# Kernel optimization log

Hardware: AMD Instinct MI355X
Metric: run time of the kernel (lower is better)

Reference implementation:

```python
import jax, jax.numpy as jnp
import numpy as np

K_SIM_SCHEDULE = [4, 8, 16]
K_CON_SCHEDULE = [2, 4, 8]
NEG = 1000000000.0


def _dual_adjacency(h, k_sim, k_con):
    """Binary causal dual adjacency (similar / dissimilar), no gradient."""
    B, T, D = h.shape
    h = jax.lax.stop_gradient(h)
    xn = h / jnp.maximum(jnp.linalg.norm(h, axis=-1, keepdims=True), 1e-12)
    sim = jnp.einsum('btd,bsd->bts', xn, xn)                 # (B,T,T)
    past = jnp.tril(jnp.ones((T, T), h.dtype), -1)           # strictly-past mask
    sim = sim * past - NEG * (1.0 - past)
    eff_sim = min(k_sim, T - 1)
    eff_con = min(k_con, max(0, T - 1 - eff_sim))
    bI = jnp.arange(B)[:, None, None]
    tI = jnp.arange(T)[None, :, None]
    A_sim = jnp.zeros((B, T, T), h.dtype)
    if eff_sim > 0:
        _, top_idx = jax.lax.top_k(sim, eff_sim)             # (B,T,k)
        A_sim = A_sim.at[bI, tI, top_idx].set(1.0) * past
    A_con = jnp.zeros((B, T, T), h.dtype)
    if eff_con > 0:
        sim_con = jnp.where(A_sim > 0, NEG, sim)
        _, bot_idx = jax.lax.top_k(-sim_con, eff_con)        # smallest eff_con
        A_con = A_con.at[bI, tI, bot_idx].set(1.0) * past * (1.0 - A_sim)
    return A_sim, A_con


def _aggregate(h, A):
    # unweighted mean over selected neighbors; empty rows -> zeros
    deg = jnp.sum(A, axis=-1, keepdims=True)
    return jnp.einsum('bts,bsd->btd', A, h) / jnp.maximum(deg, 1.0)


def setup_inputs() -> dict:
    key = jax.random.key(0)
    ks = jax.random.split(key, 2)
    B, T, D, R = 4, 2048, 512, 3
    x = jax.random.normal(ks[0], (B, T, D), dtype=jnp.float32)
    gain = jnp.ones((R, D), dtype=jnp.float32)
    bias = jnp.zeros((R, D), dtype=jnp.float32)
    log_mix = jnp.zeros((R,), dtype=jnp.float32)
    log_alpha = jnp.zeros((R,), dtype=jnp.float32)
    log_momentum = jnp.asarray(1.0, dtype=jnp.float32)
    log_scale = jnp.asarray(0.0, dtype=jnp.float32)
    return {"x": x, "gain": gain, "bias": bias, "log_mix": log_mix,
            "log_alpha": log_alpha, "log_momentum": log_momentum,
            "log_scale": log_scale}


def reference(x, gain, bias, log_mix, log_alpha, log_momentum, log_scale):
    momentum = jax.nn.sigmoid(log_momentum)
    scale = jax.nn.softplus(log_scale) + 0.01
    h = x
    for r in range(len(K_SIM_SCHEDULE)):
        mix = jax.nn.sigmoid(log_mix[r])
        alpha = jax.nn.sigmoid(log_alpha[r])
        A_sim, A_con = _dual_adjacency(h, K_SIM_SCHEDULE[r], K_CON_SCHEDULE[r])
        msg_pos = _aggregate(h, A_sim)
        msg_neg = _aggregate(h, A_con)
        ctx = alpha * msg_pos + (1.0 - alpha) * msg_neg
        blended = mix * h + (1.0 - mix) * ctx
        h_new = jax.nn.gelu(blended * gain[r] + bias[r], approximate=False)
        h = momentum * h + (1.0 - momentum) * h_new
    return (h - x) * scale
```

## Files before the change

kernel.cpp:

```cpp
#include <hip/hip_runtime.h>
#include <hip/hip_bf16.h>
#include <cstdint>
#include <cstddef>

#define BB 4
#define TT 2048
#define DD 512
#define NEG_INF (-3.402823466e+38f)
#define POS_INF (3.402823466e+38f)

typedef __attribute__((ext_vector_type(8))) short bf16x8;
typedef __attribute__((ext_vector_type(8))) unsigned short ushort8;
typedef __attribute__((ext_vector_type(4))) float f32x4;

__device__ __forceinline__ float sigmoidf_(float x){ return 1.0f/(1.0f+expf(-x)); }

__device__ __forceinline__ unsigned short f2bf(float x){
  __hip_bfloat16 b = __float2bfloat16(x);
  return *reinterpret_cast<unsigned short*>(&b);
}

__device__ __forceinline__ unsigned int fwd_map(float f){
  unsigned int b = __float_as_uint(f);
  return b ^ ((b & 0x80000000u) ? 0xFFFFFFFFu : 0x80000000u);
}
__device__ __forceinline__ float inv_map(unsigned int u){
  unsigned int b = (u & 0x80000000u) ? (u ^ 0x80000000u) : ~u;
  return __uint_as_float(b);
}

__device__ __forceinline__ unsigned long long shfl_xor64(unsigned long long x, int off){
  unsigned int hi = __shfl_xor((unsigned int)(x >> 32), off);
  unsigned int lo = __shfl_xor((unsigned int)x, off);
  return ((unsigned long long)hi << 32) | lo;
}

__global__ __launch_bounds__(64) void k_normsplit(const float* __restrict__ h, float* __restrict__ rnorm,
                                                  unsigned short* __restrict__ Xh, unsigned short* __restrict__ Xl){
  int row = blockIdx.x;
  const float* hr = h + (size_t)row*DD;
  int lane = threadIdx.x;
  float4 v0 = *(const float4*)&hr[lane*4];
  float4 v1 = *(const float4*)&hr[lane*4 + 256];
  float ss = v0.x*v0.x+v0.y*v0.y+v0.z*v0.z+v0.w*v0.w
           + v1.x*v1.x+v1.y*v1.y+v1.z*v1.z+v1.w*v1.w;
  #pragma unroll
  for (int off=32; off; off>>=1) ss += __shfl_xor(ss, off);
  float rn = 1.0f / fmaxf(sqrtf(ss), 1e-12f);
  if (lane==0) rnorm[row] = rn;

  float xs[8] = {v0.x,v0.y,v0.z,v0.w,v1.x,v1.y,v1.z,v1.w};
  unsigned short hb[8], lb[8];
  #pragma unroll
  for (int q=0;q<8;q++){
    float xn = xs[q]*rn;
    unsigned short hh = f2bf(xn);
    __hip_bfloat16 bh = *reinterpret_cast<__hip_bfloat16*>(&hh);
    float rem = xn - __bfloat162float(bh);
    hb[q] = hh; lb[q] = f2bf(rem);
  }
  ushort4 h0 = {hb[0],hb[1],hb[2],hb[3]}, h1 = {hb[4],hb[5],hb[6],hb[7]};
  ushort4 l0 = {lb[0],lb[1],lb[2],lb[3]}, l1 = {lb[4],lb[5],lb[6],lb[7]};
  *(ushort4*)&Xh[(size_t)row*DD + lane*4]       = h0;
  *(ushort4*)&Xh[(size_t)row*DD + lane*4 + 256] = h1;
  *(ushort4*)&Xl[(size_t)row*DD + lane*4]       = l0;
  *(ushort4*)&Xl[(size_t)row*DD + lane*4 + 256] = l1;
}

__global__ __launch_bounds__(256) void k_sim(const unsigned short* __restrict__ Xh,
                                             const unsigned short* __restrict__ Xl,
                                             float* __restrict__ sim, int b0){
  int p = blockIdx.x;
  int jt = (int)((sqrtf(8.0f*(float)p + 1.0f) - 1.0f)*0.5f);
  while ((jt+1)*(jt+2)/2 <= p) jt++;
  while (jt*(jt+1)/2 > p) jt--;
  int is = p - jt*(jt+1)/2;

  int bl = blockIdx.y;
  size_t xoff = (size_t)(b0 + bl)*TT*DD;
  const unsigned short* XhB = Xh + xoff;
  const unsigned short* XlB = Xl + xoff;
  float* simb = sim + (size_t)bl*TT*TT;
  int t0 = jt*128, s0 = is*128;

  __shared__ __align__(16) short As[128*32];
  __shared__ __align__(16) short Bs[128*32];

  int tid = threadIdx.x, wave = tid>>6, lane = tid&63;
  int wr = wave>>1, wc = wave&1;

  int srow = tid>>2;
  int sc8  = (tid&3)*8;

  f32x4 acc[4][4];
  #pragma unroll
  for (int m=0;m<4;m++)
    #pragma unroll
    for (int n=0;n<4;n++) acc[m][n] = (f32x4){0.f,0.f,0.f,0.f};

  ushort8 ra0, ra1, rb0, rb1;
  auto gload = [&](int s){
    int pass = s>>4; int kcol = (s&15)*32;
    const unsigned short* sA = (pass<2) ? XhB : XlB;
    const unsigned short* sB = (pass!=1) ? XhB : XlB;
    ra0 = *(const ushort8*)&sA[(size_t)(t0+srow)*DD + kcol + sc8];
    ra1 = *(const ushort8*)&sA[(size_t)(t0+srow+64)*DD + kcol + sc8];
    rb0 = *(const ushort8*)&sB[(size_t)(s0+srow)*DD + kcol + sc8];
    rb1 = *(const ushort8*)&sB[(size_t)(s0+srow+64)*DD + kcol + sc8];
  };

  gload(0);
  for (int s=0; s<48; ++s){
    __syncthreads();
    *(ushort8*)&As[srow*32 + sc8]      = ra0;
    *(ushort8*)&As[(srow+64)*32 + sc8] = ra1;
    *(ushort8*)&Bs[srow*32 + sc8]      = rb0;
    *(ushort8*)&Bs[(srow+64)*32 + sc8] = rb1;
    __syncthreads();
    if (s < 47) gload(s+1);

    int arow = wr*64 + (lane&15);
    int brow = wc*64 + (lane&15);
    int kb = (lane>>4)*8;
    bf16x8 af[4], bf[4];
    #pragma unroll
    for (int m=0;m<4;m++) af[m] = *(const bf16x8*)&As[(arow + m*16)*32 + kb];
    #pragma unroll
    for (int n=0;n<4;n++) bf[n] = *(const bf16x8*)&Bs[(brow + n*16)*32 + kb];
    #pragma unroll
    for (int m=0;m<4;m++)
      #pragma unroll
      for (int n=0;n<4;n++)
        acc[m][n] = __builtin_amdgcn_mfma_f32_16x16x32_bf16(af[m], bf[n], acc[m][n], 0, 0, 0);
  }

  #pragma unroll
  for (int m=0;m<4;m++){
    int t = t0 + wr*64 + m*16 + (lane>>4)*4;
    #pragma unroll
    for (int n=0;n<4;n++){
      int sc = s0 + wc*64 + n*16 + (lane&15);
      float* dst = simb + (size_t)t*TT + sc;
      #pragma unroll
      for (int j=0;j<4;j++) dst[(size_t)j*TT] = acc[m][n][j];
    }
  }
}

#define BMASK 0xFFFFFF00u
#define MKKEY(F,S) ((((unsigned long long)fwd_map(F)) << 32) | (unsigned int)(~(S)))
#define INS(KK) do{ unsigned long long a=(KK); \
  if (a > kv3){ \
    if (a > kv0){ unsigned long long tq=kv0; kv0=a; a=tq; } \
    if (a > kv1){ unsigned long long tq=kv1; kv1=a; a=tq; } \
    if (a > kv2){ unsigned long long tq=kv2; kv2=a; a=tq; } \
    kv3=a; } }while(0)

__device__ __forceinline__ unsigned int radix24(const float* __restrict__ srow, int t, int k1,
                                                unsigned int flip, int* sh, int lane){
  #pragma unroll
  for (int i=0;i<4;i++) sh[lane + i*64] = 0;
  int t4 = t & ~3;
  for (int s4 = lane*4; s4 < t4; s4 += 256){
    float4 f = *(const float4*)&srow[s4];
    unsigned int u0=fwd_map(f.x)^flip, u1=fwd_map(f.y)^flip, u2=fwd_map(f.z)^flip, u3=fwd_map(f.w)^flip;
    atomicAdd(&sh[u0>>24],1); atomicAdd(&sh[u1>>24],1);
    atomicAdd(&sh[u2>>24],1); atomicAdd(&sh[u3>>24],1);
  }
  for (int s = t4 + lane; s < t; s += 64){
    unsigned int u = fwd_map(srow[s])^flip;
    atomicAdd(&sh[u>>24],1);
  }
  unsigned int pfx = 0u; int kp = k1;
  #pragma unroll
  for (int pass = 0; pass < 3; ++pass){
    int shift = 24 - 8*pass;
    int m4 = sh[4*lane] + sh[4*lane+1] + sh[4*lane+2] + sh[4*lane+3];
    int x = __shfl(m4, 63-lane);
    #pragma unroll
    for (int off = 1; off < 64; off <<= 1){
      int v = __shfl_up(x, off);
      if (lane >= off) x += v;
    }
    int T = __shfl(x, 63-lane);
    int G = T - m4;
    bool hit = (G < kp) && (kp <= T);
    unsigned int npfx = 0u; int nkp = 0;
    if (hit){
      int c = G; int D = 4*lane;
      #pragma unroll
      for (int i = 3; i >= 0; --i){
        int hc = sh[4*lane + i];
        if (kp <= c + hc){ D = 4*lane + i; break; }
        c += hc;
      }
      npfx = pfx | ((unsigned int)D << shift);
      nkp = kp - c;
    }
    unsigned long long hm = __ballot(hit);
    int src = __ffsll(hm) - 1;
    pfx = __shfl(npfx, src);
    kp  = __shfl(nkp, src);
    if (pass == 2) break;

    int nshift = shift - 8;
    unsigned int keep = 0xFFFFFFFFu << shift;
    #pragma unroll
    for (int i=0;i<4;i++) sh[lane + i*64] = 0;
    for (int s4 = lane*4; s4 < t4; s4 += 256){
      float4 f = *(const float4*)&srow[s4];
      unsigned int u0=fwd_map(f.x)^flip, u1=fwd_map(f.y)^flip, u2=fwd_map(f.z)^flip, u3=fwd_map(f.w)^flip;
      if (((u0 ^ pfx) & keep) == 0) atomicAdd(&sh[(u0>>nshift)&255],1);
      if (((u1 ^ pfx) & keep) == 0) atomicAdd(&sh[(u1>>nshift)&255],1);
      if (((u2 ^ pfx) & keep) == 0) atomicAdd(&sh[(u2>>nshift)&255],1);
      if (((u3 ^ pfx) & keep) == 0) atomicAdd(&sh[(u3>>nshift)&255],1);
    }
    for (int s = t4 + lane; s < t; s += 64){
      unsigned int u = fwd_map(srow[s])^flip;
      if (((u ^ pfx) & keep) == 0) atomicAdd(&sh[(u>>nshift)&255],1);
    }
  }
  return pfx;
}

template<int ESIM, int ECON>
__global__ __launch_bounds__(256) void k_topk(const float* __restrict__ sim, int b0,
                                              const float* __restrict__ h, const float* __restrict__ rnorm,
                                              int* __restrict__ topidx, int* __restrict__ botidx,
                                              int* __restrict__ bcnt){
  constexpr int K1  = ESIM + 8;
  constexpr int K1B = ESIM + ECON + 8;
  constexpr int CANDCAP = 40;
  constexpr int EQCAP = 44;
  constexpr float TAU = 5e-5f;
  __shared__ int s_hist[4][256];
  __shared__ int s_cand[4][CANDCAP];
  __shared__ int s_eq[4][EQCAP];
  __shared__ int s_sel[4][ESIM];
  __shared__ int s_bot[4][16];
  __shared__ int s_cnt[4][2];

  int tid = threadIdx.x, lane = tid & 63, wid = tid >> 6;
  int lrow = blockIdx.x*4 + wid;
  int bl = lrow >> 11, t = lrow & (TT-1);
  int gb = b0 + bl;
  int grow = (gb << 11) | t;

  if (t <= ESIM){
    if (lane < t) topidx[(size_t)grow*16 + lane] = lane;
    if (lane == 0) bcnt[grow] = 0;
    return;
  }
  const float* srow = sim + (size_t)lrow*TT;
  const float* hb  = h + (size_t)gb*TT*DD;
  const float* rnb = rnorm + (size_t)gb*TT;

  int* sh    = s_hist[wid];
  int* scand = s_cand[wid];
  int* seq   = s_eq[wid];
  int* ssel  = s_sel[wid];
  int* sbot  = s_bot[wid];
  int t4 = t & ~3;

  unsigned long long kv0=0, kv1=0, kv2=0, kv3=0;
  {
    int s4 = lane*4;
    for (; s4 + 772 <= t4; s4 += 1024){
      float4 f0 = *(const float4*)&srow[s4];
      float4 f1 = *(const float4*)&srow[s4+256];
      float4 f2 = *(const float4*)&srow[s4+512];
      float4 f3 = *(const float4*)&srow[s4+768];
      INS(MKKEY(f0.x,s4));     INS(MKKEY(f0.y,s4+1));   INS(MKKEY(f0.z,s4+2));   INS(MKKEY(f0.w,s4+3));
      INS(MKKEY(f1.x,s4+256)); INS(MKKEY(f1.y,s4+257)); INS(MKKEY(f1.z,s4+258)); INS(MKKEY(f1.w,s4+259));
      INS(MKKEY(f2.x,s4+512)); INS(MKKEY(f2.y,s4+513)); INS(MKKEY(f2.z,s4+514)); INS(MKKEY(f2.w,s4+515));
      INS(MKKEY(f3.x,s4+768)); INS(MKKEY(f3.y,s4+769)); INS(MKKEY(f3.z,s4+770)); INS(MKKEY(f3.w,s4+771));
    }
    for (; s4 < t4; s4 += 256){
      float4 f = *(const float4*)&srow[s4];
      INS(MKKEY(f.x,s4)); INS(MKKEY(f.y,s4+1)); INS(MKKEY(f.z,s4+2)); INS(MKKEY(f.w,s4+3));
    }
    for (int s = t4 + lane; s < t; s += 64) INS(MKKEY(srow[s],s));
  }

  unsigned long long cert = kv3;
  #pragma unroll
  for (int off=32; off; off>>=1){
    unsigned long long oc = shfl_xor64(cert, off);
    if (oc > cert) cert = oc;
  }

  int myidx = 0x7fffffff;
  float vA = 0.f, vB = 0.f;
  unsigned long long keyLast = 0ull;
  #pragma unroll
  for (int k = 0; k <= ESIM; ++k){
    unsigned long long bk = kv0;
    #pragma unroll
    for (int off=32; off; off>>=1){
      unsigned long long ok = shfl_xor64(bk, off);
      if (ok > bk) bk = ok;
    }
    if (kv0 == bk){ kv0=kv1; kv1=kv2; kv2=kv3; kv3=0ull; }
    if (lane == k) myidx = (int)(~(unsigned int)bk);
    if (k == ESIM-1) vA = inv_map((unsigned int)(bk >> 32));
    if (k == ESIM){ vB = inv_map((unsigned int)(bk >> 32)); keyLast = bk; }
  }

  bool fb = (cert > keyLast) || (vA - vB < TAU);
  if (!fb){
    if (lane < ESIM){
      ssel[lane] = myidx;
      topidx[(size_t)grow*16 + lane] = myidx;
    }
  } else {
    int k1 = min(t, K1);
    unsigned int thr = radix24(srow, t, k1, 0u, sh, lane);

    if (lane == 0){ s_cnt[wid][0] = 0; s_cnt[wid][1] = 0; }
    for (int s4 = lane*4; s4 < t4; s4 += 256){
      float4 f = *(const float4*)&srow[s4];
      unsigned int uu[4] = {fwd_map(f.x), fwd_map(f.y), fwd_map(f.z), fwd_map(f.w)};
      #pragma unroll
      for (int q=0;q<4;q++){
        unsigned int b24 = uu[q] & BMASK;
        if (b24 > thr){ int p = atomicAdd(&s_cnt[wid][0],1); if (p < CANDCAP) scand[p] = s4+q; }
        else if (b24 == thr){ int p = atomicAdd(&s_cnt[wid][1],1); if (p < EQCAP) seq[p] = s4+q; }
      }
    }
    for (int s = t4 + lane; s < t; s += 64){
      unsigned int b24 = fwd_map(srow[s]) & BMASK;
      if (b24 > thr){ int p = atomicAdd(&s_cnt[wid][0],1); if (p < CANDCAP) scand[p] = s; }
      else if (b24 == thr){ int p = atomicAdd(&s_cnt[wid][1],1); if (p < EQCAP) seq[p] = s; }
    }
    int c_gt = min(s_cnt[wid][0], CANDCAP);
    int c_eq = min(s_cnt[wid][1], EQCAP);
    int ncand = min(c_gt + c_eq, 64);

    unsigned int myu = 0u; int myi = 0x7fffffff;
    if (lane < ncand){
      myi = (lane < c_gt) ? scand[lane] : seq[lane - c_gt];
      myu = fwd_map(srow[myi]);
    }

    float fvA = 0.f, fvB = 0.f;
    {
      unsigned int cu = myu; int ci = myi;
      #pragma unroll
      for (int k = 0; k <= ESIM; ++k){
        unsigned int bu = cu; int bi = ci;
        #pragma unroll
        for (int off=32; off; off>>=1){
          unsigned int ou = __shfl_xor(bu, off); int oi = __shfl_xor(bi, off);
          if (ou > bu || (ou == bu && oi < bi)){ bu = ou; bi = oi; }
        }
        if (k < ESIM && lane == 0) ssel[k] = bi;
        if (k == ESIM-1) fvA = inv_map(bu);
        if (k == ESIM)   fvB = inv_map(bu);
        if (ci == bi){ cu = 0u; ci = 0x7fffffff; }
      }
    }

    bool resc = (fvA - fvB < TAU);
    if (resc){
      const float* hq = hb + (size_t)t*DD;
      float rt = rnb[t];
      float4 q0 = *(const float4*)&hq[lane*4];
      float4 q1 = *(const float4*)&hq[lane*4 + 256];
      float ev = NEG_INF;
      for (int j = 0; j < ncand; ++j){
        int idx = (j < c_gt) ? scand[j] : seq[j - c_gt];
        const float* hc = hb + (size_t)idx*DD;
        float4 c0 = *(const float4*)&hc[lane*4];
        float4 c1 = *(const float4*)&hc[lane*4 + 256];
        float pp = q0.x*c0.x+q0.y*c0.y+q0.z*c0.z+q0.w*c0.w
                 + q1.x*c1.x+q1.y*c1.y+q1.z*c1.z+q1.w*c1.w;
        #pragma unroll
        for (int off=32; off; off>>=1) pp += __shfl_xor(pp, off);
        float ex = pp * rt * rnb[idx];
        if (lane == j) ev = ex;
      }
      float rv = (lane < ncand) ? ev : NEG_INF;
      int   ri = myi;
      #pragma unroll
      for (int k = 0; k < ESIM; ++k){
        float bv = rv; int bi = ri;
        #pragma unroll
        for (int off=32; off; off>>=1){
          float ov = __shfl_xor(bv, off); int oi = __shfl_xor(bi, off);
          if (ov > bv || (ov == bv && oi < bi)){ bv = ov; bi = oi; }
        }
        if (lane == 0) ssel[k] = bi;
        if (ri == bi) rv = NEG_INF;
      }
    }
    if (lane < ESIM) topidx[(size_t)grow*16 + lane] = ssel[lane];
  }

  int need = ECON - (TT - t);
  int cnt2 = 0;
  if (need > 0){
    constexpr unsigned int FLIP = 0xFFFFFFFFu;
    int k1b = min(t, K1B);
    unsigned int thrb = radix24(srow, t, k1b, FLIP, sh, lane);

    if (lane == 0){ s_cnt[wid][0] = 0; s_cnt[wid][1] = 0; }
    for (int s4 = lane*4; s4 < t4; s4 += 256){
      float4 f = *(const float4*)&srow[s4];
      unsigned int uu[4] = {fwd_map(f.x)^FLIP, fwd_map(f.y)^FLIP, fwd_map(f.z)^FLIP, fwd_map(f.w)^FLIP};
      #pragma unroll
      for (int q=0;q<4;q++){
        unsigned int b24 = uu[q] & BMASK;
        if (b24 > thrb){ int p = atomicAdd(&s_cnt[wid][0],1); if (p < CANDCAP) scand[p] = s4+q; }
        else if (b24 == thrb){ int p = atomicAdd(&s_cnt[wid][1],1); if (p < EQCAP) seq[p] = s4+q; }
      }
    }
    for (int s = t4 + lane; s < t; s += 64){
      unsigned int u = fwd_map(srow[s])^FLIP;
      unsigned int b24 = u & BMASK;
      if (b24 > thrb){ int p = atomicAdd(&s_cnt[wid][0],1); if (p < CANDCAP) scand[p] = s; }
      else if (b24 == thrb){ int p = atomicAdd(&s_cnt[wid][1],1); if (p < EQCAP) seq[p] = s; }
    }
    int bc_gt = min(s_cnt[wid][0], CANDCAP);
    int bc_eq = min(s_cnt[wid][1], EQCAP);
    int ncb = min(bc_gt + bc_eq, 64);

    unsigned int mu = 0u; int mi = 0x7fffffff;
    if (lane < ncb){
      mi = (lane < bc_gt) ? scand[lane] : seq[lane - bc_gt];
      mu = fwd_map(srow[mi]) ^ FLIP;
    }
    float wA = 0.f, wB = 0.f;
    unsigned int cu = mu; int ci = mi;
    #pragma unroll
    for (int k = 0; k < K1B; ++k){
      if (k < ncb && cnt2 < need + 8){
        unsigned int bu = cu; int bi = ci;
        #pragma unroll
        for (int off=32; off; off>>=1){
          unsigned int ou = __shfl_xor(bu, off); int oi = __shfl_xor(bi, off);
          if (ou > bu || (ou == bu && oi < bi)){ bu = ou; bi = oi; }
        }
        if (ci == bi){ cu = 0u; ci = 0x7fffffff; }
        bool mem = false;
        #pragma unroll
        for (int j=0;j<ESIM;j++) if (ssel[j] == bi) mem = true;
        if (!mem){
          if (lane == 0) sbot[cnt2] = bi;
          float val = inv_map(bu ^ FLIP);
          if (cnt2 == need-1) wA = val;
          if (cnt2 == need)   wB = val;
          cnt2++;
        }
      }
    }
    int npick = min(need, cnt2);
    bool rb = (cnt2 > need) && (wB - wA < TAU);
    if (!rb){
      if (lane < npick) botidx[(size_t)grow*8 + lane] = sbot[lane];
    } else {
      const float* hq = hb + (size_t)t*DD;
      float rt = rnb[t];
      float4 q0 = *(const float4*)&hq[lane*4];
      float4 q1 = *(const float4*)&hq[lane*4 + 256];
      float ev = POS_INF; int ei = 0x7fffffff;
      for (int j = 0; j < cnt2; ++j){
        int idx = sbot[j];
        const float* hc = hb + (size_t)idx*DD;
        float4 c0 = *(const float4*)&hc[lane*4];
        float4 c1 = *(const float4*)&hc[lane*4 + 256];
        float pp = q0.x*c0.x+q0.y*c0.y+q0.z*c0.z+q0.w*c0.w
                 + q1.x*c1.x+q1.y*c1.y+q1.z*c1.z+q1.w*c1.w;
        #pragma unroll
        for (int off=32; off; off>>=1) pp += __shfl_xor(pp, off);
        float ex = pp * rt * rnb[idx];
        if (lane == j){ ev = ex; ei = idx; }
      }
      #pragma unroll
      for (int k = 0; k < ECON; ++k){
        if (k < npick){
          float bv = ev; int bi = ei;
          #pragma unroll
          for (int off=32; off; off>>=1){
            float ov = __shfl_xor(bv, off); int oi = __shfl_xor(bi, off);
            if (ov < bv || (ov == bv && oi < bi)){ bv = ov; bi = oi; }
          }
          if (lane == 0) botidx[(size_t)grow*8 + k] = bi;
          if (ei == bi) ev = POS_INF;
        }
      }
    }
    cnt2 = npick;
  }
  if (lane == 0) bcnt[grow] = cnt2;
}

__global__ __launch_bounds__(256) void k_agg(const float* __restrict__ hsrc, float* __restrict__ hdst,
                                             const int* __restrict__ topidx, const int* __restrict__ botidx,
                                             const int* __restrict__ bcnt,
                                             const float* __restrict__ gain, const float* __restrict__ bias,
                                             const float* __restrict__ log_mix, const float* __restrict__ log_alpha,
                                             const float* __restrict__ log_momentum, int r, int eff_sim){
  int row = blockIdx.x;
  int b = row >> 11; int t = row & (TT-1);
  int n_sim = min(eff_sim, t);
  int n_con = bcnt[row];
  float mix      = sigmoidf_(log_mix[r]);
  float alpha    = sigmoidf_(log_alpha[r]);
  float momentum = sigmoidf_(log_momentum[0]);
  const float* hb = hsrc + (size_t)b*TT*DD;

  __shared__ int sidx[16];
  __shared__ int scidx[8];
  if (threadIdx.x < 16) sidx[threadIdx.x]  = (threadIdx.x < n_sim) ? topidx[(size_t)row*16 + threadIdx.x] : 0;
  if (threadIdx.x < 8)  scidx[threadIdx.x] = (threadIdx.x < n_con) ? botidx[(size_t)row*8  + threadIdx.x] : 0;
  __syncthreads();

  #pragma unroll
  for (int e = threadIdx.x; e < DD; e += 256){
    float sp = 0.f;
    for (int j=0;j<n_sim;j++) sp += hb[(size_t)sidx[j]*DD + e];
    float sn = 0.f;
    for (int j=0;j<n_con;j++) sn += hb[(size_t)scidx[j]*DD + e];
    float mp = sp / (float)max(n_sim, 1);
    float mn = sn / (float)max(n_con, 1);
    float ctx = alpha*mp + (1.f-alpha)*mn;
    float hv = hsrc[(size_t)row*DD + e];
    float blended = mix*hv + (1.f-mix)*ctx;
    float u = blended*gain[e] + bias[e];
    float g = 0.5f*u*(1.0f + erff(u*0.7071067811865475f));
    hdst[(size_t)row*DD + e] = momentum*hv + (1.f-momentum)*g;
  }
}

__global__ __launch_bounds__(256) void k_final(const float* __restrict__ hfin, const float* __restrict__ x,
                                               const float* __restrict__ log_scale, float* __restrict__ out, int n){
  float scale = log1pf(expf(log_scale[0])) + 0.01f;
  int i = blockIdx.x*256 + threadIdx.x;
  if (i < n) out[i] = (hfin[i] - x[i]) * scale;
}

extern "C" void kernel_launch(void* const* d_in, const int* in_sizes, int n_in,
                              void* d_out, int out_size, void* d_ws, size_t ws_size,
                              hipStream_t stream) {
  const float* x         = (const float*)d_in[0];
  const float* gain      = (const float*)d_in[1];
  const float* bias      = (const float*)d_in[2];
  const float* log_mix   = (const float*)d_in[3];
  const float* log_alpha = (const float*)d_in[4];
  const float* log_mom   = (const float*)d_in[5];
  const float* log_scale = (const float*)d_in[6];

  float* hA = (float*)d_out;
  char* ws = (char*)d_ws;
  size_t off = 0;
  auto alloc = [&](size_t bytes){ void* p = ws + off; off += (bytes + 255) & ~(size_t)255; return p; };

  float*          hB     = (float*)alloc((size_t)BB*TT*DD*4);
  float*          rnorm  = (float*)alloc((size_t)BB*TT*4);
  int*            topidx = (int*)  alloc((size_t)BB*TT*16*4);
  int*            botidx = (int*)  alloc((size_t)BB*TT*8*4);
  int*            bcnt   = (int*)  alloc((size_t)BB*TT*4);
  unsigned short* Xh     = (unsigned short*)alloc((size_t)BB*TT*DD*2);
  unsigned short* Xl     = (unsigned short*)alloc((size_t)BB*TT*DD*2);

  size_t rem = (ws_size > off) ? (ws_size - off) : 0;
  int cb = (int)(rem / ((size_t)TT*TT*4));
  if (cb < 1) cb = 1;
  if (cb > BB) cb = BB;
  float* sim = (float*)alloc((size_t)cb*TT*TT*4);

  const float* hsrc = x;
  float* hdst = hB;
  const int ks[3] = {4, 8, 16};

  for (int r = 0; r < 3; ++r){
    k_normsplit<<<BB*TT, 64, 0, stream>>>(hsrc, rnorm, Xh, Xl);
    for (int b0 = 0; b0 < BB; b0 += cb){
      int nb = (BB - b0 < cb) ? (BB - b0) : cb;
      dim3 g(136, nb);
      k_sim<<<g, 256, 0, stream>>>(Xh, Xl, sim, b0);
      if (r == 0)      k_topk<4,2><<<nb*TT/4, 256, 0, stream>>>(sim, b0, hsrc, rnorm, topidx, botidx, bcnt);
      else if (r == 1) k_topk<8,4><<<nb*TT/4, 256, 0, stream>>>(sim, b0, hsrc, rnorm, topidx, botidx, bcnt);
      else             k_topk<16,8><<<nb*TT/4, 256, 0, stream>>>(sim, b0, hsrc, rnorm, topidx, botidx, bcnt);
    }
    k_agg<<<BB*TT, 256, 0, stream>>>(hsrc, hdst, topidx, botidx, bcnt,
                                     gain + (size_t)r*DD, bias + (size_t)r*DD,
                                     log_mix, log_alpha, log_mom, r, ks[r]);
    if (r == 0){ hsrc = hB; hdst = hA; }
    else if (r == 1){ hsrc = hA; hdst = hB; }
  }
  k_final<<<(BB*TT*DD)/256, 256, 0, stream>>>(hB, x, log_scale, (float*)d_out, BB*TT*DD);
}
```

Baseline: 462.4 us.

## Emit 16-bit sort keys from sim kernel and prefilter top-k on them

Measured after the change: 467.3 us. About the same (+1.1%).

```diff
diff --git a/kernel.cpp b/kernel.cpp
--- a/kernel.cpp
+++ b/kernel.cpp
@@ -69,7 +69,8 @@
 
 __global__ __launch_bounds__(256) void k_sim(const unsigned short* __restrict__ Xh,
                                              const unsigned short* __restrict__ Xl,
-                                             float* __restrict__ sim, int b0){
+                                             float* __restrict__ sim,
+                                             unsigned short* __restrict__ keys, int b0){
   int p = blockIdx.x;
   int jt = (int)((sqrtf(8.0f*(float)p + 1.0f) - 1.0f)*0.5f);
   while ((jt+1)*(jt+2)/2 <= p) jt++;
@@ -81,6 +82,7 @@
   const unsigned short* XhB = Xh + xoff;
   const unsigned short* XlB = Xl + xoff;
   float* simb = sim + (size_t)bl*TT*TT;
+  unsigned short* keyb = keys + (size_t)bl*TT*TT;
   int t0 = jt*128, s0 = is*128;
 
   __shared__ __align__(16) short As[128*32];
@@ -141,20 +143,32 @@
     for (int n=0;n<4;n++){
       int sc = s0 + wc*64 + n*16 + (lane&15);
       float* dst = simb + (size_t)t*TT + sc;
-      #pragma unroll
-      for (int j=0;j<4;j++) dst[(size_t)j*TT] = acc[m][n][j];
+      unsigned short* kdst = keyb + (size_t)t*TT + sc;
+      #pragma unroll
+      for (int j=0;j<4;j++){
+        float v = acc[m][n][j];
+        dst[(size_t)j*TT] = v;
+        kdst[(size_t)j*TT] = (unsigned short)(fwd_map(v) >> 16);
+      }
     }
   }
 }
 
 #define BMASK 0xFFFFFF00u
-#define MKKEY(F,S) ((((unsigned long long)fwd_map(F)) << 32) | (unsigned int)(~(S)))
-#define INS(KK) do{ unsigned long long a=(KK); \
-  if (a > kv3){ \
-    if (a > kv0){ unsigned long long tq=kv0; kv0=a; a=tq; } \
-    if (a > kv1){ unsigned long long tq=kv1; kv1=a; a=tq; } \
-    if (a > kv2){ unsigned long long tq=kv2; kv2=a; a=tq; } \
-    kv3=a; } }while(0)
+
+#define KLO(D,S) ( ((D) << 16)         | (0x7FFu - (unsigned int)(S)) )
+#define KHI(D,S) ( ((D) & 0xFFFF0000u) | (0x7FFu - (unsigned int)(S)) )
+#define INS32(KK) do{ unsigned int a=(KK); \
+  if (a > kv3){ unsigned int d0=kv3; if (d0 > cert) cert = d0; \
+    if (a > kv0){ unsigned int q=kv0; kv0=a; a=q; } \
+    if (a > kv1){ unsigned int q=kv1; kv1=a; a=q; } \
+    if (a > kv2){ unsigned int q=kv2; kv2=a; a=q; } \
+    kv3=a; } \
+  else { if (a > cert) cert = a; } }while(0)
+#define PROC8(W,S) { INS32(KLO((W).x,(S)));   INS32(KHI((W).x,(S)+1)); \
+                     INS32(KLO((W).y,(S)+2)); INS32(KHI((W).y,(S)+3)); \
+                     INS32(KLO((W).z,(S)+4)); INS32(KHI((W).z,(S)+5)); \
+                     INS32(KLO((W).w,(S)+6)); INS32(KHI((W).w,(S)+7)); }
 
 __device__ __forceinline__ unsigned int radix24(const float* __restrict__ srow, int t, int k1,
                                                 unsigned int flip, int* sh, int lane){
@@ -224,7 +238,8 @@
 }
 
 template<int ESIM, int ECON>
-__global__ __launch_bounds__(256) void k_topk(const float* __restrict__ sim, int b0,
+__global__ __launch_bounds__(256) void k_topk(const float* __restrict__ sim,
+                                              const unsigned short* __restrict__ keys, int b0,
                                               const float* __restrict__ h, const float* __restrict__ rnorm,
                                               int* __restrict__ topidx, int* __restrict__ botidx,
                                               int* __restrict__ bcnt){
@@ -252,6 +267,7 @@
     return;
   }
   const float* srow = sim + (size_t)lrow*TT;
+  const unsigned short* krow = keys + (size_t)lrow*TT;
   const float* hb  = h + (size_t)gb*TT*DD;
   const float* rnb = rnorm + (size_t)gb*TT;
 
@@ -262,31 +278,55 @@
   int* sbot  = s_bot[wid];
   int t4 = t & ~3;
 
-  unsigned long long kv0=0, kv1=0, kv2=0, kv3=0;
+  unsigned int kv0=0, kv1=0, kv2=0, kv3=0, cert=0;
   {
-    int s4 = lane*4;
-    for (; s4 + 772 <= t4; s4 += 1024){
-      float4 f0 = *(const float4*)&srow[s4];
-      float4 f1 = *(const float4*)&srow[s4+256];
-      float4 f2 = *(const float4*)&srow[s4+512];
-      float4 f3 = *(const float4*)&srow[s4+768];
-      INS(MKKEY(f0.x,s4));     INS(MKKEY(f0.y,s4+1));   INS(MKKEY(f0.z,s4+2));   INS(MKKEY(f0.w,s4+3));
-      INS(MKKEY(f1.x,s4+256)); INS(MKKEY(f1.y,s4+257)); INS(MKKEY(f1.z,s4+258)); INS(MKKEY(f1.w,s4+259));
-      INS(MKKEY(f2.x,s4+512)); INS(MKKEY(f2.y,s4+513)); INS(MKKEY(f2.z,s4+514)); INS(MKKEY(f2.w,s4+515));
-      INS(MKKEY(f3.x,s4+768)); INS(MKKEY(f3.y,s4+769)); INS(MKKEY(f3.z,s4+770)); INS(MKKEY(f3.w,s4+771));
-    }
-    for (; s4 < t4; s4 += 256){
-      float4 f = *(const float4*)&srow[s4];
-      INS(MKKEY(f.x,s4)); INS(MKKEY(f.y,s4+1)); INS(MKKEY(f.z,s4+2)); INS(MKKEY(f.w,s4+3));
-    }
-    for (int s = t4 + lane; s < t; s += 64) INS(MKKEY(srow[s],s));
-  }
-
-  unsigned long long cert = kv3;
+    int nd  = t >> 1;
+    int nd4 = nd >> 2;
+    const uint4* kr4 = (const uint4*)krow;
+    uint4 w0, w1, w2, w3;
+    bool g0 = (lane       < nd4);
+    bool g1 = (lane +  64 < nd4);
+    bool g2 = (lane + 128 < nd4);
+    bool g3 = (lane + 192 < nd4);
+    if (g0) w0 = kr4[lane];
+    if (g1) w1 = kr4[lane + 64];
+    if (g2) w2 = kr4[lane + 128];
+    if (g3) w3 = kr4[lane + 192];
+    if (g0) PROC8(w0, (lane)*8);
+    if (g1) PROC8(w1, (lane+64)*8);
+    if (g2) PROC8(w2, (lane+128)*8);
+    if (g3) PROC8(w3, (lane+192)*8);
+    for (int d = nd4*4 + lane; d < nd; d += 64){
+      unsigned int w = ((const unsigned int*)krow)[d];
+      int s = 2*d;
+      INS32(KLO(w, s)); INS32(KHI(w, s+1));
+    }
+    if ((t & 1) && lane == 0){
+      unsigned int u16 = krow[t-1];
+      INS32((u16 << 16) | (0x7FFu - (unsigned int)(t-1)));
+    }
+  }
   #pragma unroll
   for (int off=32; off; off>>=1){
-    unsigned long long oc = shfl_xor64(cert, off);
+    unsigned int oc = __shfl_xor(cert, off);
     if (oc > cert) cert = oc;
+  }
+
+  unsigned long long q0=0, q1=0, q2=0, q3=0;
+  {
+    int s0i = 0x7FF - (int)(kv0 & 0xFFFFu);
+    int s1i = 0x7FF - (int)(kv1 & 0xFFFFu);
+    int s2i = 0x7FF - (int)(kv2 & 0xFFFFu);
+    int s3i = 0x7FF - (int)(kv3 & 0xFFFFu);
+    float f0=0.f, f1=0.f, f2=0.f, f3=0.f;
+    if (kv0) f0 = srow[s0i];
+    if (kv1) f1 = srow[s1i];
+    if (kv2) f2 = srow[s2i];
+    if (kv3) f3 = srow[s3i];
+    if (kv0) q0 = (((unsigned long long)fwd_map(f0)) << 32) | (unsigned int)(~s0i);
+    if (kv1) q1 = (((unsigned long long)fwd_map(f1)) << 32) | (unsigned int)(~s1i);
+    if (kv2) q2 = (((unsigned long long)fwd_map(f2)) << 32) | (unsigned int)(~s2i);
+    if (kv3) q3 = (((unsigned long long)fwd_map(f3)) << 32) | (unsigned int)(~s3i);
   }
 
   int myidx = 0x7fffffff;
@@ -294,19 +334,20 @@
   unsigned long long keyLast = 0ull;
   #pragma unroll
   for (int k = 0; k <= ESIM; ++k){
-    unsigned long long bk = kv0;
+    unsigned long long bk = q0;
     #pragma unroll
     for (int off=32; off; off>>=1){
       unsigned long long ok = shfl_xor64(bk, off);
       if (ok > bk) bk = ok;
     }
-    if (kv0 == bk){ kv0=kv1; kv1=kv2; kv2=kv3; kv3=0ull; }
+    if (q0 == bk){ q0=q1; q1=q2; q2=q3; q3=0ull; }
     if (lane == k) myidx = (int)(~(unsigned int)bk);
     if (k == ESIM-1) vA = inv_map((unsigned int)(bk >> 32));
     if (k == ESIM){ vB = inv_map((unsigned int)(bk >> 32)); keyLast = bk; }
   }
 
-  bool fb = (cert > keyLast) || (vA - vB < TAU);
+  unsigned int k16Last = (unsigned int)(keyLast >> 48);
+  bool fb = ((cert >> 16) >= k16Last) || (vA - vB < TAU);
   if (!fb){
     if (lane < ESIM){
       ssel[lane] = myidx;
@@ -364,16 +405,16 @@
     if (resc){
       const float* hq = hb + (size_t)t*DD;
       float rt = rnb[t];
-      float4 q0 = *(const float4*)&hq[lane*4];
-      float4 q1 = *(const float4*)&hq[lane*4 + 256];
+      float4 qq0 = *(const float4*)&hq[lane*4];
+      float4 qq1 = *(const float4*)&hq[lane*4 + 256];
       float ev = NEG_INF;
       for (int j = 0; j < ncand; ++j){
         int idx = (j < c_gt) ? scand[j] : seq[j - c_gt];
         const float* hc = hb + (size_t)idx*DD;
         float4 c0 = *(const float4*)&hc[lane*4];
         float4 c1 = *(const float4*)&hc[lane*4 + 256];
-        float pp = q0.x*c0.x+q0.y*c0.y+q0.z*c0.z+q0.w*c0.w
-                 + q1.x*c1.x+q1.y*c1.y+q1.z*c1.z+q1.w*c1.w;
+        float pp = qq0.x*c0.x+qq0.y*c0.y+qq0.z*c0.z+qq0.w*c0.w
+                 + qq1.x*c1.x+qq1.y*c1.y+qq1.z*c1.z+qq1.w*c1.w;
         #pragma unroll
         for (int off=32; off; off>>=1) pp += __shfl_xor(pp, off);
         float ex = pp * rt * rnb[idx];
@@ -460,16 +501,16 @@
     } else {
       const float* hq = hb + (size_t)t*DD;
       float rt = rnb[t];
-      float4 q0 = *(const float4*)&hq[lane*4];
-      float4 q1 = *(const float4*)&hq[lane*4 + 256];
+      float4 qq0 = *(const float4*)&hq[lane*4];
+      float4 qq1 = *(const float4*)&hq[lane*4 + 256];
       float ev = POS_INF; int ei = 0x7fffffff;
       for (int j = 0; j < cnt2; ++j){
         int idx = sbot[j];
         const float* hc = hb + (size_t)idx*DD;
         float4 c0 = *(const float4*)&hc[lane*4];
         float4 c1 = *(const float4*)&hc[lane*4 + 256];
-        float pp = q0.x*c0.x+q0.y*c0.y+q0.z*c0.z+q0.w*c0.w
-                 + q1.x*c1.x+q1.y*c1.y+q1.z*c1.z+q1.w*c1.w;
+        float pp = qq0.x*c0.x+qq0.y*c0.y+qq0.z*c0.z+qq0.w*c0.w
+                 + qq1.x*c1.x+qq1.y*c1.y+qq1.z*c1.z+qq1.w*c1.w;
         #pragma unroll
         for (int off=32; off; off>>=1) pp += __shfl_xor(pp, off);
         float ex = pp * rt * rnb[idx];
@@ -564,10 +605,11 @@
   unsigned short* Xl     = (unsigned short*)alloc((size_t)BB*TT*DD*2);
 
   size_t rem = (ws_size > off) ? (ws_size - off) : 0;
-  int cb = (int)(rem / ((size_t)TT*TT*4));
+  int cb = (int)(rem / ((size_t)TT*TT*6 + 512));
   if (cb < 1) cb = 1;
   if (cb > BB) cb = BB;
-  float* sim = (float*)alloc((size_t)cb*TT*TT*4);
+  float*          sim  = (float*)alloc((size_t)cb*TT*TT*4);
+  unsigned short* keys = (unsigned short*)alloc((size_t)cb*TT*TT*2);
 
   const float* hsrc = x;
   float* hdst = hB;
@@ -578,10 +620,10 @@
     for (int b0 = 0; b0 < BB; b0 += cb){
       int nb = (BB - b0 < cb) ? (BB - b0) : cb;
       dim3 g(136, nb);
-      k_sim<<<g, 256, 0, stream>>>(Xh, Xl, sim, b0);
-      if (r == 0)      k_topk<4,2><<<nb*TT/4, 256, 0, stream>>>(sim, b0, hsrc, rnorm, topidx, botidx, bcnt);
-      else if (r == 1) k_topk<8,4><<<nb*TT/4, 256, 0, stream>>>(sim, b0, hsrc, rnorm, topidx, botidx, bcnt);
-      else             k_topk<16,8><<<nb*TT/4, 256, 0, stream>>>(sim, b0, hsrc, rnorm, topidx, botidx, bcnt);
+      k_sim<<<g, 256, 0, stream>>>(Xh, Xl, sim, keys, b0);
+      if (r == 0)      k_topk<4,2><<<nb*TT/4, 256, 0, stream>>>(sim, keys, b0, hsrc, rnorm, topidx, botidx, bcnt);
+      else if (r == 1) k_topk<8,4><<<nb*TT/4, 256, 0, stream>>>(sim, keys, b0, hsrc, rnorm, topidx, botidx, bcnt);
+      else             k_topk<16,8><<<nb*TT/4, 256, 0, stream>>>(sim, keys, b0, hsrc, rnorm, topidx, botidx, bcnt);
     }
     k_agg<<<BB*TT, 256, 0, stream>>>(hsrc, hdst, topidx, botidx, bcnt,
                                      gain + (size_t)r*DD, bias + (size_t)r*DD,
```
